# Optimization experiments

Hardware: AMD Instinct MI355X
Metric: run time of the kernel (lower is better)

Reference implementation:

```python
import jax, jax.numpy as jnp
import numpy as np

B, NQ, C = 2, 10000, 256
M, L, K = 8, 3, 4
D = C // M
LEVEL_SHAPES = [(100, 100), (50, 50), (25, 25)]


def setup_inputs() -> dict:
    key = jax.random.key(0)
    ks = jax.random.split(key, 16)
    inp = {
        "query": jax.random.normal(ks[0], (B, NQ, C), jnp.float32),
        "reference_points": jax.random.uniform(ks[1], (B, NQ, 2), jnp.float32),
        "value0": jax.random.normal(ks[2], (B, C) + LEVEL_SHAPES[0], jnp.float32),
        "value1": jax.random.normal(ks[3], (B, C) + LEVEL_SHAPES[1], jnp.float32),
        "value2": jax.random.normal(ks[4], (B, C) + LEVEL_SHAPES[2], jnp.float32),
        "Wv": jax.random.normal(ks[5], (C, C), jnp.float32) * 0.02,
        "bv": jnp.zeros((C,), jnp.float32),
        "Ws": jax.random.normal(ks[6], (M * L * K * 2, C), jnp.float32) * 0.05,
        "bs": jax.random.normal(ks[7], (M * L * K * 2,), jnp.float32),
        "Wa": jax.random.normal(ks[8], (M * L * K, C), jnp.float32) * 0.02,
        "ba": jnp.zeros((M * L * K,), jnp.float32),
        "Wo": jax.random.normal(ks[9], (C, C), jnp.float32) * 0.02,
        "bo": jnp.zeros((C,), jnp.float32),
    }
    return inp


def _bilinear_sample(vflat, px, py, H, W):
    """grid_sample bilinear, align_corners=False, padding_mode='zeros'.
    vflat: (B, M, H*W, D); px, py: (B, M, Q, K) pixel coords. -> (B, M, Q, K, D)
    """
    b, m, q, k = px.shape
    x0 = jnp.floor(px)
    y0 = jnp.floor(py)
    wx1 = px - x0  # frac weights (grad 1 w.r.t. px, matching grid_sample)
    wy1 = py - y0
    wx0 = 1.0 - wx1
    wy0 = 1.0 - wy1

    def gather(xi, yi):
        valid = ((xi >= 0) & (xi <= W - 1) & (yi >= 0) & (yi <= H - 1)).astype(vflat.dtype)
        xc = jnp.clip(xi, 0, W - 1).astype(jnp.int32)
        yc = jnp.clip(yi, 0, H - 1).astype(jnp.int32)
        idx = (yc * W + xc).reshape(b, m, q * k)
        g = jnp.take_along_axis(vflat, idx[..., None], axis=2)  # (B,M,QK,D)
        return g.reshape(b, m, q, k, -1) * valid[..., None]

    out = (gather(x0, y0) * (wx0 * wy0)[..., None]
           + gather(x0 + 1, y0) * (wx1 * wy0)[..., None]
           + gather(x0, y0 + 1) * (wx0 * wy1)[..., None]
           + gather(x0 + 1, y0 + 1) * (wx1 * wy1)[..., None])
    return out


def reference(query, reference_points, value0, value1, value2,
              Wv, bv, Ws, bs, Wa, ba, Wo, bo):
    bsz, nq, c = query.shape
    dt = query.dtype
    # sampling offsets and attention weights
    off = (query @ Ws.T + bs).reshape(bsz, nq, M, L, K, 2)
    attn = jax.nn.softmax((query @ Wa.T + ba).reshape(bsz, nq, M, L * K), axis=-1)
    attn = attn.reshape(bsz, nq, M, L, K)

    out = jnp.zeros((bsz, nq, M, D), dt)
    for li, v in enumerate([value0, value1, value2]):
        H, W = v.shape[2], v.shape[3]
        # conv1x1 value projection -> per-head maps (B, M, H*W, D)
        proj = jnp.einsum('bchw,oc->bohw', v, Wv) + bv[None, :, None, None]
        vflat = proj.reshape(bsz, M, D, H * W).transpose(0, 1, 3, 2)
        norm = jnp.asarray([W, H], dt)
        loc = reference_points[:, :, None, None, :] + off[:, :, :, li, :, :] / norm  # (B,Q,M,K,2)
        # grid = loc*2-1; pixel = (grid+1)*size/2 - 0.5 = loc*size - 0.5
        px = (loc[..., 0] * W - 0.5).transpose(0, 2, 1, 3)  # (B,M,Q,K)
        py = (loc[..., 1] * H - 0.5).transpose(0, 2, 1, 3)
        sampled = _bilinear_sample(vflat, px, py, H, W)  # (B,M,Q,K,D)
        out = out + jnp.einsum('bmqkd,bqmk->bqmd', sampled, attn[:, :, :, li, :])

    out = out.reshape(bsz, nq, c)
    return out @ Wo.T + bo
```

## Files before the change

### kernel.cpp

```cpp
#include <hip/hip_runtime.h>
#include <cstddef>

#define B_ 2
#define NQ_ 10000
#define C_ 256
#define M_ 8
#define L_ 3
#define K_ 4
#define D_ 32
#define P_ 13125

typedef unsigned short u16;
typedef __attribute__((ext_vector_type(8))) short short8;
typedef __attribute__((ext_vector_type(4))) float f32x4;

static __device__ __forceinline__ u16 f2bf(float f) {
    union { float f; unsigned u; } x; x.f = f;
    unsigned r = x.u + 0x7fffu + ((x.u >> 16) & 1u);
    return (u16)(r >> 16);
}
static __device__ __forceinline__ float bf2f(u16 u) {
    union { unsigned u; float f; } x; x.u = (unsigned)u << 16;
    return x.f;
}
static __device__ __forceinline__ short8 cvt8(const float4& a, const float4& b) {
    short8 r;
    r[0] = (short)f2bf(a.x); r[1] = (short)f2bf(a.y);
    r[2] = (short)f2bf(a.z); r[3] = (short)f2bf(a.w);
    r[4] = (short)f2bf(b.x); r[5] = (short)f2bf(b.y);
    r[6] = (short)f2bf(b.z); r[7] = (short)f2bf(b.w);
    return r;
}

__global__ __launch_bounds__(256) void transpose_value(
    const float* __restrict__ v0, const float* __restrict__ v1,
    const float* __restrict__ v2, u16* __restrict__ Vt)
{
    constexpr int HWs[3]  = {10000, 2500, 625};
    constexpr int offs[3] = {0, 10000, 12500};

    const int z   = blockIdx.z;
    const int b   = z / 3;
    const int lvl = z % 3;
    const int HW  = HWs[lvl];
    const int p0  = blockIdx.x * 64;
    if (p0 >= HW) return;
    const int c0  = blockIdx.y * 64;

    const float* V = (lvl == 0 ? v0 : (lvl == 1 ? v1 : v2)) + (size_t)b * 256 * HW;

    __shared__ u16 tile[64][66];
    const int t  = threadIdx.x;
    const int pl = t & 63;
    const int cb = t >> 6;

    #pragma unroll
    for (int i = 0; i < 16; ++i) {
        int c = cb + i * 4;
        float vv = 0.f;
        if (p0 + pl < HW)
            vv = V[(size_t)(c0 + c) * HW + p0 + pl];
        tile[pl][c] = f2bf(vv);
    }
    __syncthreads();

    const int cl = t & 63;
    const int pb = t >> 6;
    #pragma unroll
    for (int i = 0; i < 16; ++i) {
        int p = pb + i * 4;
        if (p0 + p < HW)
            Vt[((size_t)b * P_ + offs[lvl] + p0 + p) * 256 + c0 + cl] = tile[p][cl];
    }
}

template <bool AF32, typename OutT>
__global__ __launch_bounds__(256) void gemm_panel(
    const void* __restrict__ Av, int rows, int nRowTiles, int npanel,
    const float* __restrict__ B1f, const float* __restrict__ bias1, int N1,
    const float* __restrict__ B2f, const float* __restrict__ bias2, int Ntot,
    OutT* __restrict__ Cout)
{
    __shared__ u16 Bs[64 * 264];

    const int bid  = blockIdx.x;
    const int rlo  = bid & 7;
    const int tmp  = bid >> 3;
    const int panel = tmp % npanel;
    const int rowTile = (tmp / npanel) * 8 + rlo;
    if (rowTile >= nRowTiles) return;

    const int t  = threadIdx.x;
    const int w  = t >> 6;
    const int l  = t & 63;
    const int row0 = rowTile * 128 + w * 32;
    const int o0   = panel * 64;
    const int lr = l & 15;
    const int kb = (l >> 4) * 8;

    #pragma unroll
    for (int i = 0; i < 8; ++i) {
        int idx = i * 256 + t;
        int col = idx >> 5;
        int kc  = (idx & 31) * 8;
        int colg = min(o0 + col, Ntot - 1);
        const float* Br = ((colg < N1) ? B1f + (size_t)colg * 256
                                       : B2f + (size_t)(colg - N1) * 256) + kc;
        float4 f0 = *reinterpret_cast<const float4*>(Br);
        float4 f1 = *reinterpret_cast<const float4*>(Br + 4);
        *reinterpret_cast<short8*>(&Bs[col * 264 + kc]) = cvt8(f0, f1);
    }

    const int ra0 = min(row0 + lr,      rows - 1);
    const int ra1 = min(row0 + 16 + lr, rows - 1);

    __syncthreads();

    f32x4 acc[2][4] = {};

    if constexpr (AF32) {
        const float* Af  = (const float*)Av;
        const float* Ap0 = Af + (size_t)ra0 * 256 + kb;
        const float* Ap1 = Af + (size_t)ra1 * 256 + kb;
        #pragma unroll
        for (int k0 = 0; k0 < 256; k0 += 32) {
            float4 x0 = *reinterpret_cast<const float4*>(Ap0 + k0);
            float4 y0 = *reinterpret_cast<const float4*>(Ap0 + k0 + 4);
            float4 x1 = *reinterpret_cast<const float4*>(Ap1 + k0);
            float4 y1 = *reinterpret_cast<const float4*>(Ap1 + k0 + 4);
            short8 a0 = cvt8(x0, y0);
            short8 a1 = cvt8(x1, y1);
            short8 b0 = *reinterpret_cast<const short8*>(&Bs[(0 * 16 + lr) * 264 + kb + k0]);
            short8 b1 = *reinterpret_cast<const short8*>(&Bs[(1 * 16 + lr) * 264 + kb + k0]);
            short8 b2 = *reinterpret_cast<const short8*>(&Bs[(2 * 16 + lr) * 264 + kb + k0]);
            short8 b3 = *reinterpret_cast<const short8*>(&Bs[(3 * 16 + lr) * 264 + kb + k0]);
            acc[0][0] = __builtin_amdgcn_mfma_f32_16x16x32_bf16(a0, b0, acc[0][0], 0, 0, 0);
            acc[0][1] = __builtin_amdgcn_mfma_f32_16x16x32_bf16(a0, b1, acc[0][1], 0, 0, 0);
            acc[0][2] = __builtin_amdgcn_mfma_f32_16x16x32_bf16(a0, b2, acc[0][2], 0, 0, 0);
            acc[0][3] = __builtin_amdgcn_mfma_f32_16x16x32_bf16(a0, b3, acc[0][3], 0, 0, 0);
            acc[1][0] = __builtin_amdgcn_mfma_f32_16x16x32_bf16(a1, b0, acc[1][0], 0, 0, 0);
            acc[1][1] = __builtin_amdgcn_mfma_f32_16x16x32_bf16(a1, b1, acc[1][1], 0, 0, 0);
            acc[1][2] = __builtin_amdgcn_mfma_f32_16x16x32_bf16(a1, b2, acc[1][2], 0, 0, 0);
            acc[1][3] = __builtin_amdgcn_mfma_f32_16x16x32_bf16(a1, b3, acc[1][3], 0, 0, 0);
        }
    } else {
        const u16* Af  = (const u16*)Av;
        const u16* Ap0 = Af + (size_t)ra0 * 256 + kb;
        const u16* Ap1 = Af + (size_t)ra1 * 256 + kb;
        #pragma unroll
        for (int k0 = 0; k0 < 256; k0 += 32) {
            short8 a0 = *reinterpret_cast<const short8*>(Ap0 + k0);
            short8 a1 = *reinterpret_cast<const short8*>(Ap1 + k0);
            short8 b0 = *reinterpret_cast<const short8*>(&Bs[(0 * 16 + lr) * 264 + kb + k0]);
            short8 b1 = *reinterpret_cast<const short8*>(&Bs[(1 * 16 + lr) * 264 + kb + k0]);
            short8 b2 = *reinterpret_cast<const short8*>(&Bs[(2 * 16 + lr) * 264 + kb + k0]);
            short8 b3 = *reinterpret_cast<const short8*>(&Bs[(3 * 16 + lr) * 264 + kb + k0]);
            acc[0][0] = __builtin_amdgcn_mfma_f32_16x16x32_bf16(a0, b0, acc[0][0], 0, 0, 0);
            acc[0][1] = __builtin_amdgcn_mfma_f32_16x16x32_bf16(a0, b1, acc[0][1], 0, 0, 0);
            acc[0][2] = __builtin_amdgcn_mfma_f32_16x16x32_bf16(a0, b2, acc[0][2], 0, 0, 0);
            acc[0][3] = __builtin_amdgcn_mfma_f32_16x16x32_bf16(a0, b3, acc[0][3], 0, 0, 0);
            acc[1][0] = __builtin_amdgcn_mfma_f32_16x16x32_bf16(a1, b0, acc[1][0], 0, 0, 0);
            acc[1][1] = __builtin_amdgcn_mfma_f32_16x16x32_bf16(a1, b1, acc[1][1], 0, 0, 0);
            acc[1][2] = __builtin_amdgcn_mfma_f32_16x16x32_bf16(a1, b2, acc[1][2], 0, 0, 0);
            acc[1][3] = __builtin_amdgcn_mfma_f32_16x16x32_bf16(a1, b3, acc[1][3], 0, 0, 0);
        }
    }

    const int orow = (l >> 4) * 4;
    #pragma unroll
    for (int ct = 0; ct < 4; ++ct) {
        const int col = o0 + ct * 16 + lr;
        if (col >= Ntot) continue;
        const float bsv = (col < N1) ? bias1[col] : bias2[col - N1];
        #pragma unroll
        for (int rt = 0; rt < 2; ++rt) {
            #pragma unroll
            for (int r = 0; r < 4; ++r) {
                const int row = row0 + rt * 16 + orow + r;
                if (row < rows) {
                    float val = acc[rt][ct][r] + bsv;
                    if constexpr (sizeof(OutT) == 2)
                        Cout[(size_t)row * Ntot + col] = (OutT)f2bf(val);
                    else
                        Cout[(size_t)row * Ntot + col] = (OutT)val;
                }
            }
        }
    }
}

__global__ __launch_bounds__(256) void sample_kernel(
    const float* __restrict__ S,
    const float* __restrict__ refp,
    const u16* __restrict__ proj,
    u16* __restrict__ out2)
{
    constexpr int Wd[3]   = {100, 50, 25};
    constexpr int offs[3] = {0, 10000, 12500};

    __shared__ int   midx[192][4];
    __shared__ float mw[192][4];

    const int t = threadIdx.x;

    if (t < 192) {
        const int q  = t / 96;
        const int tq = t % 96;
        const int tm = tq / 12;
        const int tj = tq % 12;
        const int bq = blockIdx.x * 2 + q;
        const float* Sq = S + (size_t)bq * 288;

        float lg[12], mx = -1e30f;
        #pragma unroll
        for (int jj = 0; jj < 12; ++jj) {
            lg[jj] = Sq[192 + tm * 12 + jj];
            mx = fmaxf(mx, lg[jj]);
        }
        float sum = 0.f;
        #pragma unroll
        for (int jj = 0; jj < 12; ++jj) sum += __expf(lg[jj] - mx);
        const float attn = __expf(lg[tj] - mx) / sum;

        const int l  = tj >> 2;
        const int Wl = Wd[l];
        const float refx = refp[(size_t)bq * 2 + 0];
        const float refy = refp[(size_t)bq * 2 + 1];
        const float ox = Sq[(tm * 12 + tj) * 2 + 0];
        const float oy = Sq[(tm * 12 + tj) * 2 + 1];
        const float px = refx * (float)Wl + ox - 0.5f;
        const float py = refy * (float)Wl + oy - 0.5f;
        const float x0f = floorf(px), y0f = floorf(py);
        const float wx1 = px - x0f, wy1 = py - y0f;
        const float wx0 = 1.f - wx1, wy0 = 1.f - wy1;
        const int x0 = (int)x0f, y0 = (int)y0f;
        const int x1 = x0 + 1, y1 = y0 + 1;
        const bool vx0 = (unsigned)x0 < (unsigned)Wl;
        const bool vx1 = (unsigned)x1 < (unsigned)Wl;
        const bool vy0 = (unsigned)y0 < (unsigned)Wl;
        const bool vy1 = (unsigned)y1 < (unsigned)Wl;
        const int chb  = tm * 32;
        const int base = offs[l];
        midx[t][0] = (vx0 && vy0) ? ((base + y0 * Wl + x0) * 256 + chb) : 0;
        midx[t][1] = (vx1 && vy0) ? ((base + y0 * Wl + x1) * 256 + chb) : 0;
        midx[t][2] = (vx0 && vy1) ? ((base + y1 * Wl + x0) * 256 + chb) : 0;
        midx[t][3] = (vx1 && vy1) ? ((base + y1 * Wl + x1) * 256 + chb) : 0;
        mw[t][0] = (vx0 && vy0) ? attn * wx0 * wy0 : 0.f;
        mw[t][1] = (vx1 && vy0) ? attn * wx1 * wy0 : 0.f;
        mw[t][2] = (vx0 && vy1) ? attn * wx0 * wy1 : 0.f;
        mw[t][3] = (vx1 && vy1) ? attn * wx1 * wy1 : 0.f;
    }
    __syncthreads();

    const int qi  = t >> 7;
    const int tt  = t & 127;
    const int mh  = tt >> 4;
    const int d16 = tt & 15;
    const int bq2 = blockIdx.x * 2 + qi;
    const int b   = bq2 / NQ_;
    const u16* projb = proj + (size_t)b * P_ * 256 + 2 * d16;

    float acc0 = 0.f, acc1 = 0.f;

    #pragma unroll
    for (int j = 0; j < 12; ++j) {
        const int mj = qi * 96 + mh * 12 + j;
        const int4   o  = *reinterpret_cast<const int4*>(midx[mj]);
        const float4 ww = *reinterpret_cast<const float4*>(mw[mj]);
        const unsigned u00 = *reinterpret_cast<const unsigned*>(projb + o.x);
        const unsigned u10 = *reinterpret_cast<const unsigned*>(projb + o.y);
        const unsigned u01 = *reinterpret_cast<const unsigned*>(projb + o.z);
        const unsigned u11 = *reinterpret_cast<const unsigned*>(projb + o.w);
        union { unsigned u; float f; } c0, c1;
        c0.u = u00 << 16;          c1.u = u00 & 0xffff0000u;
        acc0 = fmaf(ww.x, c0.f, acc0); acc1 = fmaf(ww.x, c1.f, acc1);
        c0.u = u10 << 16;          c1.u = u10 & 0xffff0000u;
        acc0 = fmaf(ww.y, c0.f, acc0); acc1 = fmaf(ww.y, c1.f, acc1);
        c0.u = u01 << 16;          c1.u = u01 & 0xffff0000u;
        acc0 = fmaf(ww.z, c0.f, acc0); acc1 = fmaf(ww.z, c1.f, acc1);
        c0.u = u11 << 16;          c1.u = u11 & 0xffff0000u;
        acc0 = fmaf(ww.w, c0.f, acc0); acc1 = fmaf(ww.w, c1.f, acc1);
    }

    const unsigned packed = (unsigned)f2bf(acc0) | ((unsigned)f2bf(acc1) << 16);
    *reinterpret_cast<unsigned*>(out2 + (size_t)bq2 * 256 + mh * 32 + 2 * d16) = packed;
}

extern "C" void kernel_launch(void* const* d_in, const int* in_sizes, int n_in,
                              void* d_out, int out_size, void* d_ws, size_t ws_size,
                              hipStream_t stream)
{
    const float* query = (const float*)d_in[0];
    const float* refp  = (const float*)d_in[1];
    const float* v0    = (const float*)d_in[2];
    const float* v1    = (const float*)d_in[3];
    const float* v2    = (const float*)d_in[4];
    const float* Wv    = (const float*)d_in[5];
    const float* bv    = (const float*)d_in[6];
    const float* Ws    = (const float*)d_in[7];
    const float* bs    = (const float*)d_in[8];
    const float* Wa    = (const float*)d_in[9];
    const float* ba    = (const float*)d_in[10];
    const float* Wo    = (const float*)d_in[11];
    const float* bo    = (const float*)d_in[12];
    float* out = (float*)d_out;

    char* wsb = (char*)d_ws;
    u16*   proj  = (u16*)wsb;    wsb += (size_t)B_ * P_ * 256 * 2;
    float* S     = (float*)wsb;  wsb += (size_t)B_ * NQ_ * 288 * 4;
    u16*   Vt    = (u16*)wsb;    wsb += (size_t)B_ * P_ * 256 * 2;
    u16*   out2  = (u16*)wsb;    wsb += (size_t)B_ * NQ_ * 256 * 2;

    dim3 blk(256);

    transpose_value<<<dim3(157, 4, 6), blk, 0, stream>>>(v0, v1, v2, Vt);

    gemm_panel<false, u16><<<dim3(832), blk, 0, stream>>>(
        Vt, B_ * P_, 206, 4, Wv, bv, 256, Wv, bv, 256, proj);

    gemm_panel<true, float><<<dim3(800), blk, 0, stream>>>(
        query, B_ * NQ_, 157, 5, Ws, bs, 192, Wa, ba, 288, S);

    sample_kernel<<<dim3(NQ_), blk, 0, stream>>>(S, refp, proj, out2);

    gemm_panel<false, float><<<dim3(640), blk, 0, stream>>>(
        out2, B_ * NQ_, 157, 4, Wo, bo, 256, Wo, bo, 256, out);
}
```

Measured before the change: 202.6 us.

## Fuse value transpose into projection GEMM, pre-convert weights, vectorize sampling gathers

Replaces the separate value transpose kernel and its bf16 intermediate with a projection kernel that loads fp32 value maps, transposes them into shared memory and runs the MFMA GEMM directly. Weights are converted to bf16 once in a small kernel, so the GEMMs load bf16 weight panels instead of converting fp32 in every block. The sampling kernel now has each thread gather 8 channels with 16-byte loads across a subset of points and reduce via shuffles. The trade-off is that the fused kernel re-reads fp32 value data for each of the four output panels, and an extra launch is added for the weight conversion.

```diff
diff --git a/kernel.cpp b/kernel.cpp
--- a/kernel.cpp
+++ b/kernel.cpp
@@ -19,66 +19,124 @@
     unsigned r = x.u + 0x7fffu + ((x.u >> 16) & 1u);
     return (u16)(r >> 16);
 }
-static __device__ __forceinline__ float bf2f(u16 u) {
-    union { unsigned u; float f; } x; x.u = (unsigned)u << 16;
-    return x.f;
-}
-static __device__ __forceinline__ short8 cvt8(const float4& a, const float4& b) {
-    short8 r;
-    r[0] = (short)f2bf(a.x); r[1] = (short)f2bf(a.y);
-    r[2] = (short)f2bf(a.z); r[3] = (short)f2bf(a.w);
-    r[4] = (short)f2bf(b.x); r[5] = (short)f2bf(b.y);
-    r[6] = (short)f2bf(b.z); r[7] = (short)f2bf(b.w);
-    return r;
-}
-
-__global__ __launch_bounds__(256) void transpose_value(
+
+__global__ __launch_bounds__(256) void cvt_w(
+    const float* __restrict__ Wv, const float* __restrict__ Ws,
+    const float* __restrict__ Wa, const float* __restrict__ Wo,
+    const float* __restrict__ bs, const float* __restrict__ ba,
+    u16* __restrict__ Wvbf, u16* __restrict__ WsWabf, u16* __restrict__ Wobf,
+    float* __restrict__ biasSA)
+{
+    const int t = threadIdx.x;
+    if (blockIdx.x == 200) {
+        for (int i = t; i < 288; i += 256)
+            biasSA[i] = (i < 192) ? bs[i] : ba[i - 192];
+        return;
+    }
+    const int i4 = (blockIdx.x * 256 + t) * 4;
+    const float* src; u16* dst; int off;
+    if (i4 < 65536)       { src = Wv; dst = Wvbf; off = i4; }
+    else if (i4 < 139264) {
+        int j = i4 - 65536;
+        if (j < 49152) { src = Ws; off = j; }
+        else           { src = Wa; off = j - 49152; }
+        dst = WsWabf + (j - off);
+    }
+    else                  { src = Wo; dst = Wobf; off = i4 - 139264; }
+    float4 v = *reinterpret_cast<const float4*>(src + off);
+    ushort4 o;
+    o.x = f2bf(v.x); o.y = f2bf(v.y); o.z = f2bf(v.z); o.w = f2bf(v.w);
+    *reinterpret_cast<ushort4*>(dst + off) = o;
+}
+
+__global__ __launch_bounds__(256) void proj_fused(
     const float* __restrict__ v0, const float* __restrict__ v1,
-    const float* __restrict__ v2, u16* __restrict__ Vt)
-{
-    constexpr int HWs[3]  = {10000, 2500, 625};
-    constexpr int offs[3] = {0, 10000, 12500};
-
-    const int z   = blockIdx.z;
-    const int b   = z / 3;
-    const int lvl = z % 3;
-    const int HW  = HWs[lvl];
-    const int p0  = blockIdx.x * 64;
-    if (p0 >= HW) return;
-    const int c0  = blockIdx.y * 64;
-
+    const float* __restrict__ v2,
+    const u16* __restrict__ Wvbf, const float* __restrict__ bv,
+    u16* __restrict__ proj)
+{
+    __shared__ u16 As[64 * 258];
+    __shared__ u16 Bs[64 * 264];
+
+    const int bid = blockIdx.x;
+    const int rlo = bid & 7;
+    const int tmp = bid >> 3;
+    const int panel = tmp & 3;
+    const int rowTile = (tmp >> 2) * 8 + rlo;
+    if (rowTile >= 414) return;
+
+    const int b  = rowTile / 207;
+    const int tl = rowTile % 207;
+    int lvl, p0, HW, base;
+    if (tl < 157)      { lvl = 0; p0 = tl * 64;         HW = 10000; base = 0; }
+    else if (tl < 197) { lvl = 1; p0 = (tl - 157) * 64; HW = 2500;  base = 10000; }
+    else               { lvl = 2; p0 = (tl - 197) * 64; HW = 625;   base = 12500; }
     const float* V = (lvl == 0 ? v0 : (lvl == 1 ? v1 : v2)) + (size_t)b * 256 * HW;
 
-    __shared__ u16 tile[64][66];
-    const int t  = threadIdx.x;
-    const int pl = t & 63;
-    const int cb = t >> 6;
-
-    #pragma unroll
-    for (int i = 0; i < 16; ++i) {
-        int c = cb + i * 4;
-        float vv = 0.f;
-        if (p0 + pl < HW)
-            vv = V[(size_t)(c0 + c) * HW + p0 + pl];
-        tile[pl][c] = f2bf(vv);
+    const int t = threadIdx.x;
+    const int px  = t & 63;
+    const int pxg = min(p0 + px, HW - 1);
+    const int ch0 = t >> 6;
+    #pragma unroll
+    for (int g = 0; g < 8; ++g) {
+        float vv[8];
+        #pragma unroll
+        for (int j = 0; j < 8; ++j)
+            vv[j] = V[(size_t)(ch0 + 4 * (8 * g + j)) * HW + pxg];
+        #pragma unroll
+        for (int j = 0; j < 8; ++j)
+            As[px * 258 + ch0 + 4 * (8 * g + j)] = f2bf(vv[j]);
+    }
+    const int o0 = panel * 64;
+    #pragma unroll
+    for (int i = 0; i < 8; ++i) {
+        int idx = i * 256 + t;
+        int col = idx >> 5;
+        int kc  = (idx & 31) * 8;
+        short8 v = *reinterpret_cast<const short8*>(Wvbf + (size_t)(o0 + col) * 256 + kc);
+        *reinterpret_cast<short8*>(&Bs[col * 264 + kc]) = v;
     }
     __syncthreads();
 
-    const int cl = t & 63;
-    const int pb = t >> 6;
-    #pragma unroll
-    for (int i = 0; i < 16; ++i) {
-        int p = pb + i * 4;
-        if (p0 + p < HW)
-            Vt[((size_t)b * P_ + offs[lvl] + p0 + p) * 256 + c0 + cl] = tile[p][cl];
+    const int w  = t >> 6;
+    const int l  = t & 63;
+    const int lr = l & 15;
+    const int kb = (l >> 4) * 8;
+    const int arow = w * 16 + lr;
+
+    f32x4 acc[4] = {};
+    #pragma unroll
+    for (int k0 = 0; k0 < 256; k0 += 32) {
+        short8 a  = *reinterpret_cast<const short8*>(&As[arow * 258 + kb + k0]);
+        short8 b0 = *reinterpret_cast<const short8*>(&Bs[(0 * 16 + lr) * 264 + kb + k0]);
+        short8 b1 = *reinterpret_cast<const short8*>(&Bs[(1 * 16 + lr) * 264 + kb + k0]);
+        short8 b2 = *reinterpret_cast<const short8*>(&Bs[(2 * 16 + lr) * 264 + kb + k0]);
+        short8 b3 = *reinterpret_cast<const short8*>(&Bs[(3 * 16 + lr) * 264 + kb + k0]);
+        acc[0] = __builtin_amdgcn_mfma_f32_16x16x32_bf16(a, b0, acc[0], 0, 0, 0);
+        acc[1] = __builtin_amdgcn_mfma_f32_16x16x32_bf16(a, b1, acc[1], 0, 0, 0);
+        acc[2] = __builtin_amdgcn_mfma_f32_16x16x32_bf16(a, b2, acc[2], 0, 0, 0);
+        acc[3] = __builtin_amdgcn_mfma_f32_16x16x32_bf16(a, b3, acc[3], 0, 0, 0);
+    }
+
+    const int orow = (l >> 4) * 4;
+    #pragma unroll
+    for (int ct = 0; ct < 4; ++ct) {
+        const int col = o0 + ct * 16 + lr;
+        const float bsv = bv[col];
+        #pragma unroll
+        for (int r = 0; r < 4; ++r) {
+            const int prow = w * 16 + orow + r;
+            if (p0 + prow < HW)
+                proj[((size_t)b * P_ + base + p0 + prow) * 256 + col] =
+                    f2bf(acc[ct][r] + bsv);
+        }
     }
 }
 
 template <bool AF32, typename OutT>
 __global__ __launch_bounds__(256) void gemm_panel(
     const void* __restrict__ Av, int rows, int nRowTiles, int npanel,
-    const float* __restrict__ B1f, const float* __restrict__ bias1, int N1,
-    const float* __restrict__ B2f, const float* __restrict__ bias2, int Ntot,
+    const u16* __restrict__ Bw, const float* __restrict__ bias, int Ntot,
     OutT* __restrict__ Cout)
 {
     __shared__ u16 Bs[64 * 264];
@@ -104,11 +162,8 @@
         int col = idx >> 5;
         int kc  = (idx & 31) * 8;
         int colg = min(o0 + col, Ntot - 1);
-        const float* Br = ((colg < N1) ? B1f + (size_t)colg * 256
-                                       : B2f + (size_t)(colg - N1) * 256) + kc;
-        float4 f0 = *reinterpret_cast<const float4*>(Br);
-        float4 f1 = *reinterpret_cast<const float4*>(Br + 4);
-        *reinterpret_cast<short8*>(&Bs[col * 264 + kc]) = cvt8(f0, f1);
+        short8 v = *reinterpret_cast<const short8*>(Bw + (size_t)colg * 256 + kc);
+        *reinterpret_cast<short8*>(&Bs[col * 264 + kc]) = v;
     }
 
     const int ra0 = min(row0 + lr,      rows - 1);
@@ -118,52 +173,38 @@
 
     f32x4 acc[2][4] = {};
 
-    if constexpr (AF32) {
-        const float* Af  = (const float*)Av;
-        const float* Ap0 = Af + (size_t)ra0 * 256 + kb;
-        const float* Ap1 = Af + (size_t)ra1 * 256 + kb;
-        #pragma unroll
-        for (int k0 = 0; k0 < 256; k0 += 32) {
-            float4 x0 = *reinterpret_cast<const float4*>(Ap0 + k0);
-            float4 y0 = *reinterpret_cast<const float4*>(Ap0 + k0 + 4);
-            float4 x1 = *reinterpret_cast<const float4*>(Ap1 + k0);
-            float4 y1 = *reinterpret_cast<const float4*>(Ap1 + k0 + 4);
-            short8 a0 = cvt8(x0, y0);
-            short8 a1 = cvt8(x1, y1);
-            short8 b0 = *reinterpret_cast<const short8*>(&Bs[(0 * 16 + lr) * 264 + kb + k0]);
-            short8 b1 = *reinterpret_cast<const short8*>(&Bs[(1 * 16 + lr) * 264 + kb + k0]);
-            short8 b2 = *reinterpret_cast<const short8*>(&Bs[(2 * 16 + lr) * 264 + kb + k0]);
-            short8 b3 = *reinterpret_cast<const short8*>(&Bs[(3 * 16 + lr) * 264 + kb + k0]);
-            acc[0][0] = __builtin_amdgcn_mfma_f32_16x16x32_bf16(a0, b0, acc[0][0], 0, 0, 0);
-            acc[0][1] = __builtin_amdgcn_mfma_f32_16x16x32_bf16(a0, b1, acc[0][1], 0, 0, 0);
-            acc[0][2] = __builtin_amdgcn_mfma_f32_16x16x32_bf16(a0, b2, acc[0][2], 0, 0, 0);
-            acc[0][3] = __builtin_amdgcn_mfma_f32_16x16x32_bf16(a0, b3, acc[0][3], 0, 0, 0);
-            acc[1][0] = __builtin_amdgcn_mfma_f32_16x16x32_bf16(a1, b0, acc[1][0], 0, 0, 0);
-            acc[1][1] = __builtin_amdgcn_mfma_f32_16x16x32_bf16(a1, b1, acc[1][1], 0, 0, 0);
-            acc[1][2] = __builtin_amdgcn_mfma_f32_16x16x32_bf16(a1, b2, acc[1][2], 0, 0, 0);
-            acc[1][3] = __builtin_amdgcn_mfma_f32_16x16x32_bf16(a1, b3, acc[1][3], 0, 0, 0);
-        }
-    } else {
-        const u16* Af  = (const u16*)Av;
-        const u16* Ap0 = Af + (size_t)ra0 * 256 + kb;
-        const u16* Ap1 = Af + (size_t)ra1 * 256 + kb;
-        #pragma unroll
-        for (int k0 = 0; k0 < 256; k0 += 32) {
-            short8 a0 = *reinterpret_cast<const short8*>(Ap0 + k0);
-            short8 a1 = *reinterpret_cast<const short8*>(Ap1 + k0);
-            short8 b0 = *reinterpret_cast<const short8*>(&Bs[(0 * 16 + lr) * 264 + kb + k0]);
-            short8 b1 = *reinterpret_cast<const short8*>(&Bs[(1 * 16 + lr) * 264 + kb + k0]);
-            short8 b2 = *reinterpret_cast<const short8*>(&Bs[(2 * 16 + lr) * 264 + kb + k0]);
-            short8 b3 = *reinterpret_cast<const short8*>(&Bs[(3 * 16 + lr) * 264 + kb + k0]);
-            acc[0][0] = __builtin_amdgcn_mfma_f32_16x16x32_bf16(a0, b0, acc[0][0], 0, 0, 0);
-            acc[0][1] = __builtin_amdgcn_mfma_f32_16x16x32_bf16(a0, b1, acc[0][1], 0, 0, 0);
-            acc[0][2] = __builtin_amdgcn_mfma_f32_16x16x32_bf16(a0, b2, acc[0][2], 0, 0, 0);
-            acc[0][3] = __builtin_amdgcn_mfma_f32_16x16x32_bf16(a0, b3, acc[0][3], 0, 0, 0);
-            acc[1][0] = __builtin_amdgcn_mfma_f32_16x16x32_bf16(a1, b0, acc[1][0], 0, 0, 0);
-            acc[1][1] = __builtin_amdgcn_mfma_f32_16x16x32_bf16(a1, b1, acc[1][1], 0, 0, 0);
-            acc[1][2] = __builtin_amdgcn_mfma_f32_16x16x32_bf16(a1, b2, acc[1][2], 0, 0, 0);
-            acc[1][3] = __builtin_amdgcn_mfma_f32_16x16x32_bf16(a1, b3, acc[1][3], 0, 0, 0);
-        }
+    #pragma unroll
+    for (int k0 = 0; k0 < 256; k0 += 32) {
+        short8 a0, a1;
+        if constexpr (AF32) {
+            const float* Af = (const float*)Av;
+            const float* Ap0 = Af + (size_t)ra0 * 256 + kb + k0;
+            const float* Ap1 = Af + (size_t)ra1 * 256 + kb + k0;
+            float4 x0 = *reinterpret_cast<const float4*>(Ap0);
+            float4 y0 = *reinterpret_cast<const float4*>(Ap0 + 4);
+            float4 x1 = *reinterpret_cast<const float4*>(Ap1);
+            float4 y1 = *reinterpret_cast<const float4*>(Ap1 + 4);
+            a0[0]=(short)f2bf(x0.x); a0[1]=(short)f2bf(x0.y); a0[2]=(short)f2bf(x0.z); a0[3]=(short)f2bf(x0.w);
+            a0[4]=(short)f2bf(y0.x); a0[5]=(short)f2bf(y0.y); a0[6]=(short)f2bf(y0.z); a0[7]=(short)f2bf(y0.w);
+            a1[0]=(short)f2bf(x1.x); a1[1]=(short)f2bf(x1.y); a1[2]=(short)f2bf(x1.z); a1[3]=(short)f2bf(x1.w);
+            a1[4]=(short)f2bf(y1.x); a1[5]=(short)f2bf(y1.y); a1[6]=(short)f2bf(y1.z); a1[7]=(short)f2bf(y1.w);
+        } else {
+            const u16* Af = (const u16*)Av;
+            a0 = *reinterpret_cast<const short8*>(Af + (size_t)ra0 * 256 + kb + k0);
+            a1 = *reinterpret_cast<const short8*>(Af + (size_t)ra1 * 256 + kb + k0);
+        }
+        short8 b0 = *reinterpret_cast<const short8*>(&Bs[(0 * 16 + lr) * 264 + kb + k0]);
+        short8 b1 = *reinterpret_cast<const short8*>(&Bs[(1 * 16 + lr) * 264 + kb + k0]);
+        short8 b2 = *reinterpret_cast<const short8*>(&Bs[(2 * 16 + lr) * 264 + kb + k0]);
+        short8 b3 = *reinterpret_cast<const short8*>(&Bs[(3 * 16 + lr) * 264 + kb + k0]);
+        acc[0][0] = __builtin_amdgcn_mfma_f32_16x16x32_bf16(a0, b0, acc[0][0], 0, 0, 0);
+        acc[0][1] = __builtin_amdgcn_mfma_f32_16x16x32_bf16(a0, b1, acc[0][1], 0, 0, 0);
+        acc[0][2] = __builtin_amdgcn_mfma_f32_16x16x32_bf16(a0, b2, acc[0][2], 0, 0, 0);
+        acc[0][3] = __builtin_amdgcn_mfma_f32_16x16x32_bf16(a0, b3, acc[0][3], 0, 0, 0);
+        acc[1][0] = __builtin_amdgcn_mfma_f32_16x16x32_bf16(a1, b0, acc[1][0], 0, 0, 0);
+        acc[1][1] = __builtin_amdgcn_mfma_f32_16x16x32_bf16(a1, b1, acc[1][1], 0, 0, 0);
+        acc[1][2] = __builtin_amdgcn_mfma_f32_16x16x32_bf16(a1, b2, acc[1][2], 0, 0, 0);
+        acc[1][3] = __builtin_amdgcn_mfma_f32_16x16x32_bf16(a1, b3, acc[1][3], 0, 0, 0);
     }
 
     const int orow = (l >> 4) * 4;
@@ -171,7 +212,7 @@
     for (int ct = 0; ct < 4; ++ct) {
         const int col = o0 + ct * 16 + lr;
         if (col >= Ntot) continue;
-        const float bsv = (col < N1) ? bias1[col] : bias2[col - N1];
+        const float bsv = bias[col];
         #pragma unroll
         for (int rt = 0; rt < 2; ++rt) {
             #pragma unroll
@@ -252,38 +293,56 @@
     }
     __syncthreads();
 
-    const int qi  = t >> 7;
-    const int tt  = t & 127;
-    const int mh  = tt >> 4;
-    const int d16 = tt & 15;
-    const int bq2 = blockIdx.x * 2 + qi;
-    const int b   = bq2 / NQ_;
-    const u16* projb = proj + (size_t)b * P_ * 256 + 2 * d16;
-
-    float acc0 = 0.f, acc1 = 0.f;
-
-    #pragma unroll
-    for (int j = 0; j < 12; ++j) {
-        const int mj = qi * 96 + mh * 12 + j;
+    const int qi    = t >> 7;
+    const int r     = t & 127;
+    const int chunk = r >> 2;
+    const int ptg   = r & 3;
+    const int head  = chunk >> 2;
+    const int sub   = (chunk & 3) * 8;
+    const int bq2   = blockIdx.x * 2 + qi;
+    const int b     = bq2 / NQ_;
+    const u16* projb = proj + (size_t)b * P_ * 256 + sub;
+
+    float a[8] = {0.f, 0.f, 0.f, 0.f, 0.f, 0.f, 0.f, 0.f};
+
+    #pragma unroll
+    for (int jj = 0; jj < 3; ++jj) {
+        const int pt = ptg + 4 * jj;
+        const int mj = qi * 96 + head * 12 + pt;
         const int4   o  = *reinterpret_cast<const int4*>(midx[mj]);
         const float4 ww = *reinterpret_cast<const float4*>(mw[mj]);
-        const unsigned u00 = *reinterpret_cast<const unsigned*>(projb + o.x);
-        const unsigned u10 = *reinterpret_cast<const unsigned*>(projb + o.y);
-        const unsigned u01 = *reinterpret_cast<const unsigned*>(projb + o.z);
-        const unsigned u11 = *reinterpret_cast<const unsigned*>(projb + o.w);
-        union { unsigned u; float f; } c0, c1;
-        c0.u = u00 << 16;          c1.u = u00 & 0xffff0000u;
-        acc0 = fmaf(ww.x, c0.f, acc0); acc1 = fmaf(ww.x, c1.f, acc1);
-        c0.u = u10 << 16;          c1.u = u10 & 0xffff0000u;
-        acc0 = fmaf(ww.y, c0.f, acc0); acc1 = fmaf(ww.y, c1.f, acc1);
-        c0.u = u01 << 16;          c1.u = u01 & 0xffff0000u;
-        acc0 = fmaf(ww.z, c0.f, acc0); acc1 = fmaf(ww.z, c1.f, acc1);
-        c0.u = u11 << 16;          c1.u = u11 & 0xffff0000u;
-        acc0 = fmaf(ww.w, c0.f, acc0); acc1 = fmaf(ww.w, c1.f, acc1);
-    }
-
-    const unsigned packed = (unsigned)f2bf(acc0) | ((unsigned)f2bf(acc1) << 16);
-    *reinterpret_cast<unsigned*>(out2 + (size_t)bq2 * 256 + mh * 32 + 2 * d16) = packed;
+        const int* op = &o.x;
+        const float* wp = &ww.x;
+        #pragma unroll
+        for (int c = 0; c < 4; ++c) {
+            const int4 raw = *reinterpret_cast<const int4*>(projb + op[c]);
+            const unsigned* u = reinterpret_cast<const unsigned*>(&raw);
+            const float wgt = wp[c];
+            #pragma unroll
+            for (int i = 0; i < 4; ++i) {
+                union { unsigned q; float f; } lo, hi;
+                lo.q = u[i] << 16;
+                hi.q = u[i] & 0xffff0000u;
+                a[2 * i]     = fmaf(wgt, lo.f, a[2 * i]);
+                a[2 * i + 1] = fmaf(wgt, hi.f, a[2 * i + 1]);
+            }
+        }
+    }
+
+    #pragma unroll
+    for (int i = 0; i < 8; ++i) {
+        a[i] += __shfl_xor(a[i], 1);
+        a[i] += __shfl_xor(a[i], 2);
+    }
+
+    if (ptg == 0) {
+        uint4 p;
+        p.x = (unsigned)f2bf(a[0]) | ((unsigned)f2bf(a[1]) << 16);
+        p.y = (unsigned)f2bf(a[2]) | ((unsigned)f2bf(a[3]) << 16);
+        p.z = (unsigned)f2bf(a[4]) | ((unsigned)f2bf(a[5]) << 16);
+        p.w = (unsigned)f2bf(a[6]) | ((unsigned)f2bf(a[7]) << 16);
+        *reinterpret_cast<uint4*>(out2 + (size_t)bq2 * 256 + head * 32 + sub) = p;
+    }
 }
 
 extern "C" void kernel_launch(void* const* d_in, const int* in_sizes, int n_in,
@@ -306,23 +365,26 @@
     float* out = (float*)d_out;
 
     char* wsb = (char*)d_ws;
-    u16*   proj  = (u16*)wsb;    wsb += (size_t)B_ * P_ * 256 * 2;
-    float* S     = (float*)wsb;  wsb += (size_t)B_ * NQ_ * 288 * 4;
-    u16*   Vt    = (u16*)wsb;    wsb += (size_t)B_ * P_ * 256 * 2;
-    u16*   out2  = (u16*)wsb;    wsb += (size_t)B_ * NQ_ * 256 * 2;
+    u16*   proj   = (u16*)wsb;    wsb += (size_t)B_ * P_ * 256 * 2;
+    float* S      = (float*)wsb;  wsb += (size_t)B_ * NQ_ * 288 * 4;
+    u16*   out2   = (u16*)wsb;    wsb += (size_t)B_ * NQ_ * 256 * 2;
+    u16*   Wvbf   = (u16*)wsb;    wsb += 65536 * 2;
+    u16*   WsWabf = (u16*)wsb;    wsb += 73728 * 2;
+    u16*   Wobf   = (u16*)wsb;    wsb += 65536 * 2;
+    float* biasSA = (float*)wsb;  wsb += 288 * 4;
 
     dim3 blk(256);
 
-    transpose_value<<<dim3(157, 4, 6), blk, 0, stream>>>(v0, v1, v2, Vt);
-
-    gemm_panel<false, u16><<<dim3(832), blk, 0, stream>>>(
-        Vt, B_ * P_, 206, 4, Wv, bv, 256, Wv, bv, 256, proj);
+    cvt_w<<<dim3(201), blk, 0, stream>>>(Wv, Ws, Wa, Wo, bs, ba,
+                                         Wvbf, WsWabf, Wobf, biasSA);
+
+    proj_fused<<<dim3(1664), blk, 0, stream>>>(v0, v1, v2, Wvbf, bv, proj);
 
     gemm_panel<true, float><<<dim3(800), blk, 0, stream>>>(
-        query, B_ * NQ_, 157, 5, Ws, bs, 192, Wa, ba, 288, S);
+        query, B_ * NQ_, 157, 5, WsWabf, biasSA, 288, S);
 
     sample_kernel<<<dim3(NQ_), blk, 0, stream>>>(S, refp, proj, out2);
 
     gemm_panel<false, float><<<dim3(640), blk, 0, stream>>>(
-        out2, B_ * NQ_, 157, 4, Wo, bo, 256, Wo, bo, 256, out);
-}
+        out2, B_ * NQ_, 157, 4, Wobf, bo, 256, out);
+}
```

Result: slower. 217.9 us (+7.6%).

## Fuse value transpose into projection GEMM and prefetch A operands to registers

Applied to the files above, without the earlier changes.

Replaces the separate transpose kernel and value-projection GEMM with one kernel. It loads NCHW value tiles, converts them to bf16 into shared memory in transposed layout, and runs the MFMA projection directly. This removes the Vt intermediate round trip and one launch. Each block handles 64 pixels by 64 output channels, so every input tile is re-read once per output panel (4 times). Separately, the generic GEMM now loads all A-row fragments into registers before staging B, so the global loads overlap the B fill, at the cost of more registers.

```diff
diff --git a/kernel.cpp b/kernel.cpp
--- a/kernel.cpp
+++ b/kernel.cpp
@@ -19,10 +19,6 @@
     unsigned r = x.u + 0x7fffu + ((x.u >> 16) & 1u);
     return (u16)(r >> 16);
 }
-static __device__ __forceinline__ float bf2f(u16 u) {
-    union { unsigned u; float f; } x; x.u = (unsigned)u << 16;
-    return x.f;
-}
 static __device__ __forceinline__ short8 cvt8(const float4& a, const float4& b) {
     short8 r;
     r[0] = (short)f2bf(a.x); r[1] = (short)f2bf(a.y);
@@ -32,45 +28,89 @@
     return r;
 }
 
-__global__ __launch_bounds__(256) void transpose_value(
+__global__ __launch_bounds__(256) void proj_fused(
     const float* __restrict__ v0, const float* __restrict__ v1,
-    const float* __restrict__ v2, u16* __restrict__ Vt)
+    const float* __restrict__ v2,
+    const float* __restrict__ Wv, const float* __restrict__ bv,
+    u16* __restrict__ proj)
 {
-    constexpr int HWs[3]  = {10000, 2500, 625};
-    constexpr int offs[3] = {0, 10000, 12500};
-
-    const int z   = blockIdx.z;
-    const int b   = z / 3;
-    const int lvl = z % 3;
-    const int HW  = HWs[lvl];
-    const int p0  = blockIdx.x * 64;
-    if (p0 >= HW) return;
-    const int c0  = blockIdx.y * 64;
-
+    __shared__ u16 As[64 * 264];
+    __shared__ u16 Bs[64 * 264];
+
+    const int bid = blockIdx.x;
+    const int rlo = bid & 7;
+    const int tmp = bid >> 3;
+    const int panel = tmp & 3;
+    const int rowTile = (tmp >> 2) * 8 + rlo;
+    if (rowTile >= 414) return;
+
+    const int b  = rowTile / 207;
+    const int tl = rowTile % 207;
+    int lvl, p0, HW, base;
+    if (tl < 157)      { lvl = 0; p0 = tl * 64;         HW = 10000; base = 0; }
+    else if (tl < 197) { lvl = 1; p0 = (tl - 157) * 64; HW = 2500;  base = 10000; }
+    else               { lvl = 2; p0 = (tl - 197) * 64; HW = 625;   base = 12500; }
     const float* V = (lvl == 0 ? v0 : (lvl == 1 ? v1 : v2)) + (size_t)b * 256 * HW;
 
-    __shared__ u16 tile[64][66];
-    const int t  = threadIdx.x;
-    const int pl = t & 63;
-    const int cb = t >> 6;
-
-    #pragma unroll
-    for (int i = 0; i < 16; ++i) {
-        int c = cb + i * 4;
-        float vv = 0.f;
-        if (p0 + pl < HW)
-            vv = V[(size_t)(c0 + c) * HW + p0 + pl];
-        tile[pl][c] = f2bf(vv);
+    const int t = threadIdx.x;
+    const int px  = t & 63;
+    const int pxg = min(p0 + px, HW - 1);
+    const int ch0 = t >> 6;
+    #pragma unroll
+    for (int g = 0; g < 8; ++g) {
+        float vv[8];
+        #pragma unroll
+        for (int j = 0; j < 8; ++j)
+            vv[j] = V[(size_t)(ch0 + 4 * (8 * g + j)) * HW + pxg];
+        #pragma unroll
+        for (int j = 0; j < 8; ++j)
+            As[px * 264 + ch0 + 4 * (8 * g + j)] = f2bf(vv[j]);
+    }
+    const int o0 = panel * 64;
+    #pragma unroll
+    for (int i = 0; i < 8; ++i) {
+        int idx = i * 256 + t;
+        int col = idx >> 5;
+        int kc  = (idx & 31) * 8;
+        const float* Br = Wv + (size_t)(o0 + col) * 256 + kc;
+        float4 f0 = *reinterpret_cast<const float4*>(Br);
+        float4 f1 = *reinterpret_cast<const float4*>(Br + 4);
+        *reinterpret_cast<short8*>(&Bs[col * 264 + kc]) = cvt8(f0, f1);
     }
     __syncthreads();
 
-    const int cl = t & 63;
-    const int pb = t >> 6;
-    #pragma unroll
-    for (int i = 0; i < 16; ++i) {
-        int p = pb + i * 4;
-        if (p0 + p < HW)
-            Vt[((size_t)b * P_ + offs[lvl] + p0 + p) * 256 + c0 + cl] = tile[p][cl];
+    const int w  = t >> 6;
+    const int l  = t & 63;
+    const int lr = l & 15;
+    const int kb = (l >> 4) * 8;
+    const int arow = w * 16 + lr;
+
+    f32x4 acc[4] = {};
+    #pragma unroll
+    for (int k0 = 0; k0 < 256; k0 += 32) {
+        short8 a  = *reinterpret_cast<const short8*>(&As[arow * 264 + kb + k0]);
+        short8 b0 = *reinterpret_cast<const short8*>(&Bs[(0 * 16 + lr) * 264 + kb + k0]);
+        short8 b1 = *reinterpret_cast<const short8*>(&Bs[(1 * 16 + lr) * 264 + kb + k0]);
+        short8 b2 = *reinterpret_cast<const short8*>(&Bs[(2 * 16 + lr) * 264 + kb + k0]);
+        short8 b3 = *reinterpret_cast<const short8*>(&Bs[(3 * 16 + lr) * 264 + kb + k0]);
+        acc[0] = __builtin_amdgcn_mfma_f32_16x16x32_bf16(a, b0, acc[0], 0, 0, 0);
+        acc[1] = __builtin_amdgcn_mfma_f32_16x16x32_bf16(a, b1, acc[1], 0, 0, 0);
+        acc[2] = __builtin_amdgcn_mfma_f32_16x16x32_bf16(a, b2, acc[2], 0, 0, 0);
+        acc[3] = __builtin_amdgcn_mfma_f32_16x16x32_bf16(a, b3, acc[3], 0, 0, 0);
+    }
+
+    const int orow = (l >> 4) * 4;
+    #pragma unroll
+    for (int ct = 0; ct < 4; ++ct) {
+        const int col = o0 + ct * 16 + lr;
+        const float bsv = bv[col];
+        #pragma unroll
+        for (int r = 0; r < 4; ++r) {
+            const int prow = w * 16 + orow + r;
+            if (p0 + prow < HW)
+                proj[((size_t)b * P_ + base + p0 + prow) * 256 + col] =
+                    f2bf(acc[ct][r] + bsv);
+        }
     }
 }
 
@@ -97,6 +137,34 @@
     const int o0   = panel * 64;
     const int lr = l & 15;
     const int kb = (l >> 4) * 8;
+
+    const int ra0 = min(row0 + lr,      rows - 1);
+    const int ra1 = min(row0 + 16 + lr, rows - 1);
+
+    short8 a0r[8], a1r[8];
+    if constexpr (AF32) {
+        const float* Af  = (const float*)Av;
+        const float* Ap0 = Af + (size_t)ra0 * 256 + kb;
+        const float* Ap1 = Af + (size_t)ra1 * 256 + kb;
+        #pragma unroll
+        for (int s = 0; s < 8; ++s) {
+            float4 x0 = *reinterpret_cast<const float4*>(Ap0 + s * 32);
+            float4 y0 = *reinterpret_cast<const float4*>(Ap0 + s * 32 + 4);
+            float4 x1 = *reinterpret_cast<const float4*>(Ap1 + s * 32);
+            float4 y1 = *reinterpret_cast<const float4*>(Ap1 + s * 32 + 4);
+            a0r[s] = cvt8(x0, y0);
+            a1r[s] = cvt8(x1, y1);
+        }
+    } else {
+        const u16* Af  = (const u16*)Av;
+        const u16* Ap0 = Af + (size_t)ra0 * 256 + kb;
+        const u16* Ap1 = Af + (size_t)ra1 * 256 + kb;
+        #pragma unroll
+        for (int s = 0; s < 8; ++s) {
+            a0r[s] = *reinterpret_cast<const short8*>(Ap0 + s * 32);
+            a1r[s] = *reinterpret_cast<const short8*>(Ap1 + s * 32);
+        }
+    }
 
     #pragma unroll
     for (int i = 0; i < 8; ++i) {
@@ -110,60 +178,25 @@
         float4 f1 = *reinterpret_cast<const float4*>(Br + 4);
         *reinterpret_cast<short8*>(&Bs[col * 264 + kc]) = cvt8(f0, f1);
     }
-
-    const int ra0 = min(row0 + lr,      rows - 1);
-    const int ra1 = min(row0 + 16 + lr, rows - 1);
-
     __syncthreads();
 
     f32x4 acc[2][4] = {};
 
-    if constexpr (AF32) {
-        const float* Af  = (const float*)Av;
-        const float* Ap0 = Af + (size_t)ra0 * 256 + kb;
-        const float* Ap1 = Af + (size_t)ra1 * 256 + kb;
-        #pragma unroll
-        for (int k0 = 0; k0 < 256; k0 += 32) {
-            float4 x0 = *reinterpret_cast<const float4*>(Ap0 + k0);
-            float4 y0 = *reinterpret_cast<const float4*>(Ap0 + k0 + 4);
-            float4 x1 = *reinterpret_cast<const float4*>(Ap1 + k0);
-            float4 y1 = *reinterpret_cast<const float4*>(Ap1 + k0 + 4);
-            short8 a0 = cvt8(x0, y0);
-            short8 a1 = cvt8(x1, y1);
-            short8 b0 = *reinterpret_cast<const short8*>(&Bs[(0 * 16 + lr) * 264 + kb + k0]);
-            short8 b1 = *reinterpret_cast<const short8*>(&Bs[(1 * 16 + lr) * 264 + kb + k0]);
-            short8 b2 = *reinterpret_cast<const short8*>(&Bs[(2 * 16 + lr) * 264 + kb + k0]);
-            short8 b3 = *reinterpret_cast<const short8*>(&Bs[(3 * 16 + lr) * 264 + kb + k0]);
-            acc[0][0] = __builtin_amdgcn_mfma_f32_16x16x32_bf16(a0, b0, acc[0][0], 0, 0, 0);
-            acc[0][1] = __builtin_amdgcn_mfma_f32_16x16x32_bf16(a0, b1, acc[0][1], 0, 0, 0);
-            acc[0][2] = __builtin_amdgcn_mfma_f32_16x16x32_bf16(a0, b2, acc[0][2], 0, 0, 0);
-            acc[0][3] = __builtin_amdgcn_mfma_f32_16x16x32_bf16(a0, b3, acc[0][3], 0, 0, 0);
-            acc[1][0] = __builtin_amdgcn_mfma_f32_16x16x32_bf16(a1, b0, acc[1][0], 0, 0, 0);
-            acc[1][1] = __builtin_amdgcn_mfma_f32_16x16x32_bf16(a1, b1, acc[1][1], 0, 0, 0);
-            acc[1][2] = __builtin_amdgcn_mfma_f32_16x16x32_bf16(a1, b2, acc[1][2], 0, 0, 0);
-            acc[1][3] = __builtin_amdgcn_mfma_f32_16x16x32_bf16(a1, b3, acc[1][3], 0, 0, 0);
-        }
-    } else {
-        const u16* Af  = (const u16*)Av;
-        const u16* Ap0 = Af + (size_t)ra0 * 256 + kb;
-        const u16* Ap1 = Af + (size_t)ra1 * 256 + kb;
-        #pragma unroll
-        for (int k0 = 0; k0 < 256; k0 += 32) {
-            short8 a0 = *reinterpret_cast<const short8*>(Ap0 + k0);
-            short8 a1 = *reinterpret_cast<const short8*>(Ap1 + k0);
-            short8 b0 = *reinterpret_cast<const short8*>(&Bs[(0 * 16 + lr) * 264 + kb + k0]);
-            short8 b1 = *reinterpret_cast<const short8*>(&Bs[(1 * 16 + lr) * 264 + kb + k0]);
-            short8 b2 = *reinterpret_cast<const short8*>(&Bs[(2 * 16 + lr) * 264 + kb + k0]);
-            short8 b3 = *reinterpret_cast<const short8*>(&Bs[(3 * 16 + lr) * 264 + kb + k0]);
-            acc[0][0] = __builtin_amdgcn_mfma_f32_16x16x32_bf16(a0, b0, acc[0][0], 0, 0, 0);
-            acc[0][1] = __builtin_amdgcn_mfma_f32_16x16x32_bf16(a0, b1, acc[0][1], 0, 0, 0);
-            acc[0][2] = __builtin_amdgcn_mfma_f32_16x16x32_bf16(a0, b2, acc[0][2], 0, 0, 0);
-            acc[0][3] = __builtin_amdgcn_mfma_f32_16x16x32_bf16(a0, b3, acc[0][3], 0, 0, 0);
-            acc[1][0] = __builtin_amdgcn_mfma_f32_16x16x32_bf16(a1, b0, acc[1][0], 0, 0, 0);
-            acc[1][1] = __builtin_amdgcn_mfma_f32_16x16x32_bf16(a1, b1, acc[1][1], 0, 0, 0);
-            acc[1][2] = __builtin_amdgcn_mfma_f32_16x16x32_bf16(a1, b2, acc[1][2], 0, 0, 0);
-            acc[1][3] = __builtin_amdgcn_mfma_f32_16x16x32_bf16(a1, b3, acc[1][3], 0, 0, 0);
-        }
+    #pragma unroll
+    for (int s = 0; s < 8; ++s) {
+        const int k0 = s * 32;
+        short8 b0 = *reinterpret_cast<const short8*>(&Bs[(0 * 16 + lr) * 264 + kb + k0]);
+        short8 b1 = *reinterpret_cast<const short8*>(&Bs[(1 * 16 + lr) * 264 + kb + k0]);
+        short8 b2 = *reinterpret_cast<const short8*>(&Bs[(2 * 16 + lr) * 264 + kb + k0]);
+        short8 b3 = *reinterpret_cast<const short8*>(&Bs[(3 * 16 + lr) * 264 + kb + k0]);
+        acc[0][0] = __builtin_amdgcn_mfma_f32_16x16x32_bf16(a0r[s], b0, acc[0][0], 0, 0, 0);
+        acc[0][1] = __builtin_amdgcn_mfma_f32_16x16x32_bf16(a0r[s], b1, acc[0][1], 0, 0, 0);
+        acc[0][2] = __builtin_amdgcn_mfma_f32_16x16x32_bf16(a0r[s], b2, acc[0][2], 0, 0, 0);
+        acc[0][3] = __builtin_amdgcn_mfma_f32_16x16x32_bf16(a0r[s], b3, acc[0][3], 0, 0, 0);
+        acc[1][0] = __builtin_amdgcn_mfma_f32_16x16x32_bf16(a1r[s], b0, acc[1][0], 0, 0, 0);
+        acc[1][1] = __builtin_amdgcn_mfma_f32_16x16x32_bf16(a1r[s], b1, acc[1][1], 0, 0, 0);
+        acc[1][2] = __builtin_amdgcn_mfma_f32_16x16x32_bf16(a1r[s], b2, acc[1][2], 0, 0, 0);
+        acc[1][3] = __builtin_amdgcn_mfma_f32_16x16x32_bf16(a1r[s], b3, acc[1][3], 0, 0, 0);
     }
 
     const int orow = (l >> 4) * 4;
@@ -306,17 +339,13 @@
     float* out = (float*)d_out;
 
     char* wsb = (char*)d_ws;
-    u16*   proj  = (u16*)wsb;    wsb += (size_t)B_ * P_ * 256 * 2;
-    float* S     = (float*)wsb;  wsb += (size_t)B_ * NQ_ * 288 * 4;
-    u16*   Vt    = (u16*)wsb;    wsb += (size_t)B_ * P_ * 256 * 2;
-    u16*   out2  = (u16*)wsb;    wsb += (size_t)B_ * NQ_ * 256 * 2;
+    u16*   proj = (u16*)wsb;    wsb += (size_t)B_ * P_ * 256 * 2;
+    float* S    = (float*)wsb;  wsb += (size_t)B_ * NQ_ * 288 * 4;
+    u16*   out2 = (u16*)wsb;    wsb += (size_t)B_ * NQ_ * 256 * 2;
 
     dim3 blk(256);
 
-    transpose_value<<<dim3(157, 4, 6), blk, 0, stream>>>(v0, v1, v2, Vt);
-
-    gemm_panel<false, u16><<<dim3(832), blk, 0, stream>>>(
-        Vt, B_ * P_, 206, 4, Wv, bv, 256, Wv, bv, 256, proj);
+    proj_fused<<<dim3(1664), blk, 0, stream>>>(v0, v1, v2, Wv, bv, proj);
 
     gemm_panel<true, float><<<dim3(800), blk, 0, stream>>>(
         query, B_ * NQ_, 157, 5, Ws, bs, 192, Wa, ba, 288, S);
```

After: 206.1 us. About the same (+1.8%).
